# Kernel tuning notes

Hardware: AMD Instinct MI355X
Metric: run time of the kernel (lower is better)

The kernel has to match this reference:

```python
import jax, jax.numpy as jnp
import numpy as np

N = 50000
E = 800000
IN_DIM = 64          # 'in_dim'; ndata h has dim 2*in_dim, p has dim in_dim
EDGE_DIM = 32
OUT_DIM = 64
AVG_D_LOG = 2.8332   # avg_d['log'] = log(avg_degree + 1), avg_degree = 16
EPS_STD = 1e-5
EPS_BN = 1e-5


def setup_inputs() -> dict:
    key = jax.random.key(0)
    ks = jax.random.split(key, 16)
    def glorot(k, fan_in, fan_out):
        lim = np.sqrt(6.0 / (fan_in + fan_out)).astype(np.float32)
        return jax.random.uniform(k, (fan_in, fan_out), jnp.float32, -lim, lim)
    d_pre_h = 2 * 2 * IN_DIM + EDGE_DIM   # 288
    d_pre_p = 2 * IN_DIM + EDGE_DIM       # 160
    d_post_h = (4 * 3 + 2) * IN_DIM       # 896
    d_post_p = (4 * 3 + 1) * IN_DIM       # 832
    return {
        "h": jax.random.normal(ks[0], (N, 2 * IN_DIM), jnp.float32),
        "p": jax.random.normal(ks[1], (N, IN_DIM), jnp.float32),
        "e": jax.random.normal(ks[2], (E, EDGE_DIM), jnp.float32),
        "src": jax.random.randint(ks[3], (E,), 0, N, jnp.int32),
        "dst": jax.random.randint(ks[4], (E,), 0, N, jnp.int32),
        "snorm_n": jax.random.uniform(ks[5], (N, 1), jnp.float32, 0.05, 1.0),
        "W_pre_h": glorot(ks[6], d_pre_h, IN_DIM),
        "b_pre_h": jnp.zeros((IN_DIM,), jnp.float32),
        "W_pre_p": glorot(ks[7], d_pre_p, IN_DIM),
        "b_pre_p": jnp.zeros((IN_DIM,), jnp.float32),
        "W_post_h": glorot(ks[8], d_post_h, OUT_DIM),
        "b_post_h": jnp.zeros((OUT_DIM,), jnp.float32),
        "W_post_p": glorot(ks[9], d_post_p, OUT_DIM),
        "b_post_p": jnp.zeros((OUT_DIM,), jnp.float32),
        "bn_gamma": jnp.ones((OUT_DIM,), jnp.float32),
        "bn_beta": jnp.zeros((OUT_DIM,), jnp.float32),
    }


def _agg_scale(msg, dst, deg):
    # msg: [E, d] edge messages reduced at dst; PNA aggregators mean/max/min/std
    degc = jnp.maximum(deg, 1.0)
    s = jax.ops.segment_sum(msg, dst, num_segments=N)
    mean = s / degc[:, None]
    sq = jax.ops.segment_sum(msg * msg, dst, num_segments=N) / degc[:, None]
    var = jax.nn.relu(sq - mean * mean)
    std = jnp.sqrt(var + EPS_STD)
    has = (deg > 0)[:, None]
    mx = jnp.where(has, jax.ops.segment_max(msg, dst, num_segments=N), 0.0)
    mn = jnp.where(has, jax.ops.segment_min(msg, dst, num_segments=N), 0.0)
    agg = jnp.concatenate([mean, mx, mn, std], axis=1)  # [N, 4d]
    logd = jnp.where(deg > 0, jnp.log(deg + 1.0), 1.0)
    amp = (logd / AVG_D_LOG)[:, None]
    att = (AVG_D_LOG / logd)[:, None]
    # scalers: identity, amplification, attenuation -> [N, 12d]
    return jnp.concatenate([agg, agg * amp, agg * att], axis=1)


def reference(h, p, e, src, dst, snorm_n,
              W_pre_h, b_pre_h, W_pre_p, b_pre_p,
              W_post_h, b_post_h, W_post_p, b_post_p,
              bn_gamma, bn_beta):
    # pretrans (1-layer MLP == linear) on concatenated edge endpoint features
    z_h = jnp.concatenate([h[src], h[dst], e], axis=1)   # [E, 4*in+edge]
    z_p = jnp.concatenate([p[src], p[dst], e], axis=1)   # [E, 2*in+edge]
    e_for_h = z_h @ W_pre_h + b_pre_h                    # [E, in]
    e_for_p = z_p @ W_pre_p + b_pre_p                    # [E, in]

    deg = jax.ops.segment_sum(jnp.ones((E,), jnp.float32), dst, num_segments=N)
    agg_h = _agg_scale(e_for_h, dst, deg)                # [N, 12*in]
    agg_p = _agg_scale(e_for_p, dst, deg)                # [N, 12*in]

    h_cat = jnp.concatenate([h, agg_h], axis=1)          # [N, 14*in]
    p_cat = jnp.concatenate([p, agg_p], axis=1)          # [N, 13*in]
    h_out = h_cat @ W_post_h + b_post_h                  # [N, out]
    p_out = p_cat @ W_post_p + b_post_p                  # [N, out]

    # graph norm
    h_out = h_out * snorm_n
    # batch norm (training-mode batch statistics, biased variance)
    mu = jnp.mean(h_out, axis=0)
    var = jnp.mean((h_out - mu) ** 2, axis=0)
    h_out = (h_out - mu) / jnp.sqrt(var + EPS_BN) * bn_gamma + bn_beta
    # dropout = identity (eval / p=0)
    return h_out, p_out
```

## Files before the change

### kernel.cpp

```cpp
#include <hip/hip_runtime.h>
#include <hip/hip_bf16.h>
#include <hip/hip_fp16.h>


#define N_NODES 50000
#define N_EDGES 800000
#define NS 3200000
#define AVG_D_LOG 2.8332f

typedef unsigned short u16;
typedef unsigned int u32;
typedef __attribute__((ext_vector_type(8))) short short8;
typedef __attribute__((ext_vector_type(4))) float f32x4;

__device__ __forceinline__ float bflo(u32 u) { return __uint_as_float(u << 16); }
__device__ __forceinline__ float bfhi(u32 u) { return __uint_as_float(u & 0xffff0000u); }
__device__ __forceinline__ float bf2f(u16 u) { return __uint_as_float(((u32)u) << 16); }
__device__ __forceinline__ u16 f2bf(float x) {
  u32 u = __float_as_uint(x);
  return (u16)((u + 0x7fff + ((u >> 16) & 1)) >> 16);
}
__device__ __forceinline__ u16 f2h(float x) { return __half_as_ushort(__float2half(x)); }
__device__ __forceinline__ float h2f(u16 x) { return __half2float(__ushort_as_half(x)); }
__device__ __forceinline__ float hlo(u32 u) { return __half2float(__ushort_as_half((u16)(u & 0xffffu))); }
__device__ __forceinline__ float hhi(u32 u) { return __half2float(__ushort_as_half((u16)(u >> 16))); }

__device__ __forceinline__ int is_bf(const void* gamma) {
  return ((const u32*)gamma)[0] == 0x3F803F80u ? 1 : 0;
}

__device__ __forceinline__ f32x4 mfma16(short8 a, short8 b, f32x4 c) {
  return __builtin_amdgcn_mfma_f32_16x16x32_bf16(a, b, c, 0, 0, 0);
}

__device__ __forceinline__ void load8(float z[8], const void* base, size_t off,
                                      int bf) {
  if (bf) {
    uint4 u = *(const uint4*)((const u16*)base + off);
    z[0] = bflo(u.x); z[1] = bfhi(u.x); z[2] = bflo(u.y); z[3] = bfhi(u.y);
    z[4] = bflo(u.z); z[5] = bfhi(u.z); z[6] = bflo(u.w); z[7] = bfhi(u.w);
  } else {
    const float* f = (const float*)base + off;
    float4 a = *(const float4*)f;
    float4 b = *(const float4*)(f + 4);
    z[0] = a.x; z[1] = a.y; z[2] = a.z; z[3] = a.w;
    z[4] = b.x; z[5] = b.y; z[6] = b.z; z[7] = b.w;
  }
}

__device__ __forceinline__ float load1(const void* base, size_t off, int bf) {
  return bf ? bf2f(((const u16*)base)[off]) : ((const float*)base)[off];
}

__global__ __launch_bounds__(256) void k_convert(
    const void* __restrict__ Wpreh, const void* __restrict__ Wprep,
    const void* __restrict__ Wposth, const void* __restrict__ Wpostp,
    const void* __restrict__ bpreh, const void* __restrict__ bprep,
    const void* __restrict__ bposth, const void* __restrict__ bpostp,
    const void* __restrict__ gamma, float* __restrict__ bias,
    u16* __restrict__ frag) {
  int i = blockIdx.x * 256 + threadIdx.x;
  if (i >= 256 + 139264) return;
  int bf = is_bf(gamma);
  if (i < 256) {
    const void* s = (i < 64) ? bpreh : (i < 128) ? bprep : (i < 192) ? bposth : bpostp;
    bias[i] = load1(s, i & 63, bf);
    return;
  }
  int g = i - 256;
  const void* W; int fidx, rowoff;
  if (g < 8192)        { W = Wpreh;  fidx = g;          rowoff = 0; }
  else if (g < 16384)  { W = Wpreh;  fidx = g - 8192;   rowoff = 128; }
  else if (g < 20480)  { W = Wprep;  fidx = g - 16384;  rowoff = 0; }
  else if (g < 24576)  { W = Wprep;  fidx = g - 20480;  rowoff = 64; }
  else if (g < 81920)  { W = Wposth; fidx = g - 24576;  rowoff = 0; }
  else if (g < 135168) { W = Wpostp; fidx = g - 81920;  rowoff = 0; }
  else if (g < 137216) { W = Wpreh;  fidx = g - 135168; rowoff = 256; }
  else                 { W = Wprep;  fidx = g - 137216; rowoff = 128; }
  int f = fidx;
  int kc = f >> 11, nt = (f >> 9) & 3, lane = (f >> 3) & 63, j = f & 7;
  int k = kc * 32 + (lane >> 4) * 8 + j;
  int n = nt * 16 + (lane & 15);
  frag[g] = f2bf(load1(W, (size_t)(rowoff + k) * 64 + n, bf));
}

__global__ __launch_bounds__(256) void k_hist(const int* __restrict__ dst,
                                              int* __restrict__ cnt) {
  int i = blockIdx.x * 256 + threadIdx.x;
  if (i < N_EDGES) atomicAdd(cnt + dst[i], 1);
}

__global__ __launch_bounds__(1024) void k_scan1(const int* __restrict__ cnt,
                                                int* __restrict__ offs,
                                                int* __restrict__ bsum) {
  __shared__ int buf[1024];
  int t = threadIdx.x;
  int i = blockIdx.x * 1024 + t;
  int v = (i < N_NODES) ? cnt[i] : 0;
  buf[t] = v;
  __syncthreads();
#pragma unroll
  for (int d = 1; d < 1024; d <<= 1) {
    int x = (t >= d) ? buf[t - d] : 0;
    __syncthreads();
    buf[t] += x;
    __syncthreads();
  }
  if (i < N_NODES) offs[i] = buf[t] - v;
  if (t == 1023) bsum[blockIdx.x] = buf[1023];
}
__global__ void k_scan2(const int* __restrict__ bsum, int* __restrict__ boff,
                        int* __restrict__ offs, int nb) {
  if (threadIdx.x == 0 && blockIdx.x == 0) {
    int run = 0;
    for (int b = 0; b < nb; ++b) { boff[b] = run; run += bsum[b]; }
    offs[N_NODES] = run;
  }
}
__global__ __launch_bounds__(256) void k_scan3(int* __restrict__ offs,
                                               const int* __restrict__ boff,
                                               int* __restrict__ cnt) {
  int i = blockIdx.x * 256 + threadIdx.x;
  if (i < N_NODES) {
    int v = offs[i] + boff[i >> 10];
    offs[i] = v;
    cnt[i] = v;
  }
}

__global__ __launch_bounds__(256) void k_order(const int* __restrict__ src,
                                               const int* __restrict__ dst,
                                               int* __restrict__ cnt,
                                               int2* __restrict__ epack) {
  int i = blockIdx.x * 256 + threadIdx.x;
  if (i < N_EDGES) {
    int pos = atomicAdd(cnt + dst[i], 1);
    epack[pos] = make_int2(i, src[i]);
  }
}

__global__ __launch_bounds__(256) void k_uproj(
    const void* __restrict__ h, const void* __restrict__ p,
    const float* __restrict__ bias, const u16* __restrict__ frag,
    const void* __restrict__ gamma, u16* __restrict__ Usrc,
    u16* __restrict__ Udst) {
  int wid = (blockIdx.x * 256 + threadIdx.x) >> 6;
  int lane = threadIdx.x & 63;
  if (wid >= 12500) return;
  int part = wid / 3125;
  int node0 = (wid % 3125) * 16;
  int bf = is_bf(gamma);
  const void* feat = (part < 2) ? h : p;
  int pitch = (part < 2) ? 128 : 64;
  int kcn = (part < 2) ? 4 : 2;
  const u16* bfr = frag + (part == 0 ? 0 : part == 1 ? 8192 : part == 2 ? 16384 : 20480);
  u16* U = (part & 1) ? Udst : Usrc;
  int tw = part >> 1;
  int m = lane & 15, quad = lane >> 4;
  f32x4 acc[4];
#pragma unroll
  for (int nt = 0; nt < 4; ++nt) acc[nt] = (f32x4){0.f, 0.f, 0.f, 0.f};
#pragma unroll
  for (int kc = 0; kc < 4; ++kc) {
    if (kc >= kcn) break;
    float z[8];
    load8(z, feat, (size_t)(node0 + m) * pitch + kc * 32 + quad * 8, bf);
    short8 a;
#pragma unroll
    for (int q = 0; q < 8; ++q) a[q] = (short)f2bf(z[q]);
#pragma unroll
    for (int nt = 0; nt < 4; ++nt) {
      short8 b = *(const short8*)(bfr + (size_t)((kc * 4 + nt) * 64 + lane) * 8);
      acc[nt] = mfma16(a, b, acc[nt]);
    }
  }
  const float* bv = (part == 1) ? bias : (part == 3) ? bias + 64 : nullptr;
#pragma unroll
  for (int r = 0; r < 4; ++r) {
    int node = node0 + quad * 4 + r;
#pragma unroll
    for (int nt = 0; nt < 4; ++nt) {
      int col = nt * 16 + m;
      float v = acc[nt][r] + (bv ? bv[col] : 0.f);
      U[(size_t)node * 128 + col * 2 + tw] = f2h(v);
    }
  }
}

template <int BF>
__global__ __launch_bounds__(256, 4) void k_aggf(
    const void* __restrict__ e, const int2* __restrict__ epack,
    const int* __restrict__ offs, const u32* __restrict__ Us32,
    const u32* __restrict__ Ud32, const u16* __restrict__ Wfh,
    const u16* __restrict__ Wfp, const void* __restrict__ gamma,
    u16* __restrict__ Ah, u16* __restrict__ Ap, float* __restrict__ degf) {
  if (is_bf(gamma) != BF) return;
  int n = blockIdx.x * 4 + (threadIdx.x >> 6);
  int lane = threadIdx.x & 63;
  if (n >= N_NODES) return;
  int m = lane & 15, quad = lane >> 4;
  int s = offs[n], epos = offs[n + 1];
  int deg = epos - s;

  short8 bh[4], bp[4];
#pragma unroll
  for (int nt = 0; nt < 4; ++nt) {
    bh[nt] = *(const short8*)(Wfh + (size_t)(nt * 64 + lane) * 8);
    bp[nt] = *(const short8*)(Wfp + (size_t)(nt * 64 + lane) * 8);
  }
  float uhd[4], upd[4];
#pragma unroll
  for (int nt = 0; nt < 4; ++nt) {
    u32 u = Ud32[(size_t)n * 64 + nt * 16 + m];
    uhd[nt] = hlo(u); upd[nt] = hhi(u);
  }
  float hsum[4], hsq[4], hmx[4], hmn[4], psum[4], psq[4], pmx[4], pmn[4];
#pragma unroll
  for (int nt = 0; nt < 4; ++nt) {
    hsum[nt] = hsq[nt] = psum[nt] = psq[nt] = 0.f;
    hmx[nt] = pmx[nt] = -3.4e38f;
    hmn[nt] = pmn[nt] = 3.4e38f;
  }

  for (int c0 = 0; c0 < deg; c0 += 16) {
    int im = s + c0 + m; im = im < epos ? im : epos - 1;
    int eid = epack[im].x;
    int b0 = s + c0 + quad * 4;
    int i0 = b0 < epos ? b0 : epos - 1;
    int i1 = b0 + 1 < epos ? b0 + 1 : epos - 1;
    int i2 = b0 + 2 < epos ? b0 + 2 : epos - 1;
    int i3 = b0 + 3 < epos ? b0 + 3 : epos - 1;
    int sce0 = epack[i0].y, sce1 = epack[i1].y;
    int sce2 = epack[i2].y, sce3 = epack[i3].y;
    u32 usv0[4], usv1[4], usv2[4], usv3[4];
#pragma unroll
    for (int nt = 0; nt < 4; ++nt) {
      usv0[nt] = Us32[(size_t)sce0 * 64 + nt * 16 + m];
      usv1[nt] = Us32[(size_t)sce1 * 64 + nt * 16 + m];
      usv2[nt] = Us32[(size_t)sce2 * 64 + nt * 16 + m];
      usv3[nt] = Us32[(size_t)sce3 * 64 + nt * 16 + m];
    }
    float z[8];
    load8(z, e, (size_t)eid * 32 + quad * 8, BF);
    short8 a;
#pragma unroll
    for (int q = 0; q < 8; ++q) a[q] = (short)f2bf(z[q]);
    bool v0 = (c0 + quad * 4 + 0) < deg;
    bool v1 = (c0 + quad * 4 + 1) < deg;
    bool v2 = (c0 + quad * 4 + 2) < deg;
    bool v3 = (c0 + quad * 4 + 3) < deg;

    {
      f32x4 acc[4];
#pragma unroll
      for (int nt = 0; nt < 4; ++nt)
        acc[nt] = mfma16(a, bh[nt], (f32x4){0.f, 0.f, 0.f, 0.f});
#pragma unroll
      for (int nt = 0; nt < 4; ++nt) {
        float w0 = acc[nt][0] + hlo(usv0[nt]);
        float w1 = acc[nt][1] + hlo(usv1[nt]);
        float w2 = acc[nt][2] + hlo(usv2[nt]);
        float w3 = acc[nt][3] + hlo(usv3[nt]);
        hmx[nt] = fmaxf(fmaxf(hmx[nt], w0), fmaxf(fmaxf(w1, w2), w3));
        hmn[nt] = fminf(fminf(hmn[nt], w0), fminf(fminf(w1, w2), w3));
        float z0 = v0 ? w0 : 0.f, z1 = v1 ? w1 : 0.f;
        float z2 = v2 ? w2 : 0.f, z3 = v3 ? w3 : 0.f;
        hsum[nt] += (z0 + z1) + (z2 + z3);
        hsq[nt] = fmaf(z0, z0, fmaf(z1, z1, fmaf(z2, z2, fmaf(z3, z3, hsq[nt]))));
      }
    }
    {
      f32x4 acc[4];
#pragma unroll
      for (int nt = 0; nt < 4; ++nt)
        acc[nt] = mfma16(a, bp[nt], (f32x4){0.f, 0.f, 0.f, 0.f});
#pragma unroll
      for (int nt = 0; nt < 4; ++nt) {
        float w0 = acc[nt][0] + hhi(usv0[nt]);
        float w1 = acc[nt][1] + hhi(usv1[nt]);
        float w2 = acc[nt][2] + hhi(usv2[nt]);
        float w3 = acc[nt][3] + hhi(usv3[nt]);
        pmx[nt] = fmaxf(fmaxf(pmx[nt], w0), fmaxf(fmaxf(w1, w2), w3));
        pmn[nt] = fminf(fminf(pmn[nt], w0), fminf(fminf(w1, w2), w3));
        float z0 = v0 ? w0 : 0.f, z1 = v1 ? w1 : 0.f;
        float z2 = v2 ? w2 : 0.f, z3 = v3 ? w3 : 0.f;
        psum[nt] += (z0 + z1) + (z2 + z3);
        psq[nt] = fmaf(z0, z0, fmaf(z1, z1, fmaf(z2, z2, fmaf(z3, z3, psq[nt]))));
      }
    }
  }

  float dv = (float)deg;
  bool has = deg > 0;
  float inv = has ? 1.f / dv : 1.f;
  if (lane == 0) degf[n] = dv;

#pragma unroll
  for (int nt = 0; nt < 4; ++nt) {
    hsum[nt] += __shfl_xor(hsum[nt], 16); hsum[nt] += __shfl_xor(hsum[nt], 32);
    hsq[nt] += __shfl_xor(hsq[nt], 16);   hsq[nt] += __shfl_xor(hsq[nt], 32);
    hmx[nt] = fmaxf(hmx[nt], __shfl_xor(hmx[nt], 16));
    hmx[nt] = fmaxf(hmx[nt], __shfl_xor(hmx[nt], 32));
    hmn[nt] = fminf(hmn[nt], __shfl_xor(hmn[nt], 16));
    hmn[nt] = fminf(hmn[nt], __shfl_xor(hmn[nt], 32));
    psum[nt] += __shfl_xor(psum[nt], 16); psum[nt] += __shfl_xor(psum[nt], 32);
    psq[nt] += __shfl_xor(psq[nt], 16);   psq[nt] += __shfl_xor(psq[nt], 32);
    pmx[nt] = fmaxf(pmx[nt], __shfl_xor(pmx[nt], 16));
    pmx[nt] = fmaxf(pmx[nt], __shfl_xor(pmx[nt], 32));
    pmn[nt] = fminf(pmn[nt], __shfl_xor(pmn[nt], 16));
    pmn[nt] = fminf(pmn[nt], __shfl_xor(pmn[nt], 32));
  }

#pragma unroll
  for (int nt = 0; nt < 4; ++nt) {
    {
      float mean_w = hsum[nt] * inv;
      float var = fmaf(-mean_w, mean_w, hsq[nt] * inv);
      var = var > 0.f ? var : 0.f;
      float sd = sqrtf(var + 1e-5f);
      float o = quad == 0 ? (has ? mean_w + uhd[nt] : 0.f)
              : quad == 1 ? (has ? hmx[nt] + uhd[nt] : 0.f)
              : quad == 2 ? (has ? hmn[nt] + uhd[nt] : 0.f) : sd;
      Ah[(size_t)n * 256 + quad * 64 + nt * 16 + m] = f2bf(o);
    }
    {
      float mean_w = psum[nt] * inv;
      float var = fmaf(-mean_w, mean_w, psq[nt] * inv);
      var = var > 0.f ? var : 0.f;
      float sd = sqrtf(var + 1e-5f);
      float o = quad == 0 ? (has ? mean_w + upd[nt] : 0.f)
              : quad == 1 ? (has ? pmx[nt] + upd[nt] : 0.f)
              : quad == 2 ? (has ? pmn[nt] + upd[nt] : 0.f) : sd;
      Ap[(size_t)n * 256 + quad * 64 + nt * 16 + m] = f2bf(o);
    }
  }
}

__global__ __launch_bounds__(256) void k_node(
    const void* __restrict__ h, const void* __restrict__ p,
    const u16* __restrict__ Ah, const u16* __restrict__ Ap,
    const void* __restrict__ snorm, const float* __restrict__ degf,
    const u16* __restrict__ BfH, const u16* __restrict__ BfP,
    const float* __restrict__ biasH, const float* __restrict__ biasP,
    const void* __restrict__ gamma, float* __restrict__ outh,
    float* __restrict__ outp) {
  int w = (blockIdx.x * 256 + threadIdx.x) >> 6;
  int lane = threadIdx.x & 63;
  if (w >= N_NODES / 16) return;
  int bf = is_bf(gamma);
  int m = lane & 15, quad = lane >> 4;
  int node0 = w * 16;

  float ampr[4], attr[4];
#pragma unroll
  for (int r = 0; r < 4; ++r) {
    float dv = degf[node0 + quad * 4 + r];
    float logd = (dv > 0.5f) ? logf(dv + 1.f) : 1.f;
    ampr[r] = logd * (1.f / AVG_D_LOG);
    attr[r] = AVG_D_LOG / logd;
  }

  f32x4 accB[4], accA[4], accT[4];
#pragma unroll
  for (int nt = 0; nt < 4; ++nt) {
    accB[nt] = (f32x4){0.f, 0.f, 0.f, 0.f};
    accA[nt] = (f32x4){0.f, 0.f, 0.f, 0.f};
    accT[nt] = (f32x4){0.f, 0.f, 0.f, 0.f};
  }
#pragma unroll 2
  for (int kc = 0; kc < 12; ++kc) {
    short8 a;
    if (kc < 4) {
      float z[8];
      load8(z, h, (size_t)(node0 + m) * 128 + kc * 32 + quad * 8, bf);
#pragma unroll
      for (int q = 0; q < 8; ++q) a[q] = (short)f2bf(z[q]);
    } else {
      a = *(const short8*)(Ah + (size_t)(node0 + m) * 256 + (kc - 4) * 32 + quad * 8);
    }
#pragma unroll
    for (int nt = 0; nt < 4; ++nt)
      accB[nt] = mfma16(a, *(const short8*)(BfH + (size_t)((kc * 4 + nt) * 64 + lane) * 8), accB[nt]);
    if (kc >= 4) {
      int kk = kc - 4;
#pragma unroll
      for (int nt = 0; nt < 4; ++nt)
        accA[nt] = mfma16(a, *(const short8*)(BfH + 24576 + (size_t)((kk * 4 + nt) * 64 + lane) * 8), accA[nt]);
#pragma unroll
      for (int nt = 0; nt < 4; ++nt)
        accT[nt] = mfma16(a, *(const short8*)(BfH + 40960 + (size_t)((kk * 4 + nt) * 64 + lane) * 8), accT[nt]);
    }
  }
  float bH[4];
#pragma unroll
  for (int nt = 0; nt < 4; ++nt) bH[nt] = biasH[nt * 16 + m];
#pragma unroll
  for (int r = 0; r < 4; ++r) {
    int node = node0 + quad * 4 + r;
    float sn = load1(snorm, node, bf);
#pragma unroll
    for (int nt = 0; nt < 4; ++nt) {
      float v = accB[nt][r] + ampr[r] * accA[nt][r] + attr[r] * accT[nt][r] + bH[nt];
      outh[(size_t)node * 64 + nt * 16 + m] = v * sn;
    }
  }

#pragma unroll
  for (int nt = 0; nt < 4; ++nt) {
    accB[nt] = (f32x4){0.f, 0.f, 0.f, 0.f};
    accA[nt] = (f32x4){0.f, 0.f, 0.f, 0.f};
    accT[nt] = (f32x4){0.f, 0.f, 0.f, 0.f};
  }
#pragma unroll 2
  for (int kc = 0; kc < 10; ++kc) {
    short8 a;
    if (kc < 2) {
      float z[8];
      load8(z, p, (size_t)(node0 + m) * 64 + kc * 32 + quad * 8, bf);
#pragma unroll
      for (int q = 0; q < 8; ++q) a[q] = (short)f2bf(z[q]);
    } else {
      a = *(const short8*)(Ap + (size_t)(node0 + m) * 256 + (kc - 2) * 32 + quad * 8);
    }
#pragma unroll
    for (int nt = 0; nt < 4; ++nt)
      accB[nt] = mfma16(a, *(const short8*)(BfP + (size_t)((kc * 4 + nt) * 64 + lane) * 8), accB[nt]);
    if (kc >= 2) {
      int kk = kc - 2;
#pragma unroll
      for (int nt = 0; nt < 4; ++nt)
        accA[nt] = mfma16(a, *(const short8*)(BfP + 20480 + (size_t)((kk * 4 + nt) * 64 + lane) * 8), accA[nt]);
#pragma unroll
      for (int nt = 0; nt < 4; ++nt)
        accT[nt] = mfma16(a, *(const short8*)(BfP + 36864 + (size_t)((kk * 4 + nt) * 64 + lane) * 8), accT[nt]);
    }
  }
  float bP[4];
#pragma unroll
  for (int nt = 0; nt < 4; ++nt) bP[nt] = biasP[nt * 16 + m];
#pragma unroll
  for (int r = 0; r < 4; ++r) {
    int node = node0 + quad * 4 + r;
#pragma unroll
    for (int nt = 0; nt < 4; ++nt) {
      float v = accB[nt][r] + ampr[r] * accA[nt][r] + attr[r] * accT[nt][r] + bP[nt];
      outp[(size_t)node * 64 + nt * 16 + m] = v;
    }
  }
}

__global__ __launch_bounds__(256) void k_bnstats(const float* __restrict__ hpre,
                                                 float* __restrict__ bnacc) {
  int j = threadIdx.x & 63;
  float s = 0.0f, q = 0.0f;
  for (int n = blockIdx.x * 4 + (threadIdx.x >> 6); n < N_NODES;
       n += gridDim.x * 4) {
    float x = hpre[(size_t)n * 64 + j];
    s += x; q += x * x;
  }
  __shared__ float ls[256], lq[256];
  ls[threadIdx.x] = s; lq[threadIdx.x] = q;
  __syncthreads();
  if (threadIdx.x < 64) {
    s = ls[threadIdx.x] + ls[threadIdx.x + 64] + ls[threadIdx.x + 128] + ls[threadIdx.x + 192];
    q = lq[threadIdx.x] + lq[threadIdx.x + 64] + lq[threadIdx.x + 128] + lq[threadIdx.x + 192];
    atomicAdd(bnacc + threadIdx.x, s);
    atomicAdd(bnacc + 64 + threadIdx.x, q);
  }
}

__global__ __launch_bounds__(256) void k_bnapply(
    float* __restrict__ outh, const float* __restrict__ bnacc,
    const void* __restrict__ gamma, const void* __restrict__ beta) {
  int i = blockIdx.x * 256 + threadIdx.x;
  if (i >= NS) return;
  int bf = is_bf(gamma);
  int j = i & 63;
  const float invN = 1.0f / (float)N_NODES;
  float mu = bnacc[j] * invN;
  float var = fmaf(-mu, mu, bnacc[64 + j] * invN);
  var = var > 0.0f ? var : 0.0f;
  float sc = load1(gamma, j, bf) * rsqrtf(var + 1e-5f);
  float sh = load1(beta, j, bf) - mu * sc;
  outh[i] = fmaf(outh[i], sc, sh);
}

extern "C" void kernel_launch(void* const* d_in, const int* in_sizes, int n_in,
                              void* d_out, int out_size, void* d_ws,
                              size_t ws_size, hipStream_t stream) {
  const void* h = d_in[0];
  const void* p = d_in[1];
  const void* e = d_in[2];
  const int* src = (const int*)d_in[3];
  const int* dst = (const int*)d_in[4];
  const void* snorm = d_in[5];
  const void* Wpreh = d_in[6];
  const void* bpreh = d_in[7];
  const void* Wprep = d_in[8];
  const void* bprep = d_in[9];
  const void* Wposth = d_in[10];
  const void* bposth = d_in[11];
  const void* Wpostp = d_in[12];
  const void* bpostp = d_in[13];
  const void* gamma = d_in[14];
  const void* beta = d_in[15];

  float* ws = (float*)d_ws;
  u16* Usrc = (u16*)ws;
  u16* Udst = (u16*)(ws + 3200000L);
  u16* Ah = (u16*)(ws + 6400000L);
  u16* Ap = (u16*)(ws + 12800000L);
  int2* epack = (int2*)(ws + 19200000L);
  int* cnt = (int*)(ws + 20800016L);
  int* offs = (int*)(ws + 20850016L);
  float* degf = ws + 20900020L;
  int* bsum = (int*)(ws + 20950020L);
  int* boff = (int*)(ws + 20950084L);
  float* bnacc = ws + 20950148L;
  float* bias = ws + 20950276L;
  u16* frag = (u16*)(ws + 20950532L);

  u16* fragPostH = frag + 24576;
  u16* fragPostP = frag + 81920;
  u16* fragWehF = frag + 135168;
  u16* fragWepF = frag + 137216;

  float* outh = (float*)d_out;
  float* outp = outh + (size_t)NS;

  int bfh = -1;
  if (in_sizes && n_in >= 16) {
    if (in_sizes[0] == 25600000) bfh = 0;
    else if (in_sizes[0] == 12800000) bfh = 1;
  }

  hipMemsetAsync(cnt, 0, N_NODES * sizeof(int), stream);
  hipMemsetAsync(bnacc, 0, 128 * sizeof(float), stream);
  k_convert<<<(256 + 139264 + 255) / 256, 256, 0, stream>>>(
      Wpreh, Wprep, Wposth, Wpostp, bpreh, bprep, bposth, bpostp, gamma, bias,
      frag);
  k_hist<<<(N_EDGES + 255) / 256, 256, 0, stream>>>(dst, cnt);
  const int NB = (N_NODES + 1023) / 1024;
  k_scan1<<<NB, 1024, 0, stream>>>(cnt, offs, bsum);
  k_scan2<<<1, 64, 0, stream>>>(bsum, boff, offs, NB);
  k_scan3<<<(N_NODES + 255) / 256, 256, 0, stream>>>(offs, boff, cnt);
  k_order<<<(N_EDGES + 255) / 256, 256, 0, stream>>>(src, dst, cnt, epack);
  k_uproj<<<(12500 + 3) / 4, 256, 0, stream>>>(h, p, bias, frag, gamma, Usrc,
                                               Udst);
  if (bfh != 1)
    k_aggf<0><<<(N_NODES + 3) / 4, 256, 0, stream>>>(
        e, epack, offs, (const u32*)Usrc, (const u32*)Udst, fragWehF, fragWepF,
        gamma, Ah, Ap, degf);
  if (bfh != 0)
    k_aggf<1><<<(N_NODES + 3) / 4, 256, 0, stream>>>(
        e, epack, offs, (const u32*)Usrc, (const u32*)Udst, fragWehF, fragWepF,
        gamma, Ah, Ap, degf);
  k_node<<<(N_NODES / 16 + 3) / 4, 256, 0, stream>>>(
      h, p, Ah, Ap, snorm, degf, fragPostH, fragPostP, bias + 128, bias + 192,
      gamma, outh, outp);
  k_bnstats<<<256, 256, 0, stream>>>(outh, bnacc);
  k_bnapply<<<(NS + 255) / 256, 256, 0, stream>>>(outh, bnacc, gamma, beta);
}
```

Before: 513.6 us.

## Fuse memsets and scan passes, merge h/p projections, split full edge chunks

Several changes land together. Zeroing of counts and BN accumulators moves into the weight-convert kernel, and the three-kernel scan becomes a single-block scan. The U projection computes the h and p halves in one wave and writes packed half2 words. The aggregation kernel gives each wave two nodes, handles full 16-edge chunks without clamping or masking, and loads bf16 edge features directly. Together these cut launch count and per-edge overhead, but the single-block scan runs serially on one block and the paired-node waves may lose some occupancy balance.

```diff
diff --git a/kernel.cpp b/kernel.cpp
--- a/kernel.cpp
+++ b/kernel.cpp
@@ -20,8 +20,6 @@
   u32 u = __float_as_uint(x);
   return (u16)((u + 0x7fff + ((u >> 16) & 1)) >> 16);
 }
-__device__ __forceinline__ u16 f2h(float x) { return __half_as_ushort(__float2half(x)); }
-__device__ __forceinline__ float h2f(u16 x) { return __half2float(__ushort_as_half(x)); }
 __device__ __forceinline__ float hlo(u32 u) { return __half2float(__ushort_as_half((u16)(u & 0xffffu))); }
 __device__ __forceinline__ float hhi(u32 u) { return __half2float(__ushort_as_half((u16)(u >> 16))); }
 
@@ -52,15 +50,35 @@
   return bf ? bf2f(((const u16*)base)[off]) : ((const float*)base)[off];
 }
 
+__device__ __forceinline__ short8 cvt8bf(const float z[8]) {
+  union { __hip_bfloat162 b[4]; short8 s; } u;
+  u.b[0] = __float22bfloat162_rn(make_float2(z[0], z[1]));
+  u.b[1] = __float22bfloat162_rn(make_float2(z[2], z[3]));
+  u.b[2] = __float22bfloat162_rn(make_float2(z[4], z[5]));
+  u.b[3] = __float22bfloat162_rn(make_float2(z[6], z[7]));
+  return u.s;
+}
+
+__device__ __forceinline__ u32 packh2(float a, float b) {
+  union { __half2 h; u32 u; } x;
+  x.h = __float22half2_rn(make_float2(a, b));
+  return x.u;
+}
+
 __global__ __launch_bounds__(256) void k_convert(
     const void* __restrict__ Wpreh, const void* __restrict__ Wprep,
     const void* __restrict__ Wposth, const void* __restrict__ Wpostp,
     const void* __restrict__ bpreh, const void* __restrict__ bprep,
     const void* __restrict__ bposth, const void* __restrict__ bpostp,
     const void* __restrict__ gamma, float* __restrict__ bias,
-    u16* __restrict__ frag) {
+    u16* __restrict__ frag, int* __restrict__ cnt, float* __restrict__ bnacc) {
   int i = blockIdx.x * 256 + threadIdx.x;
-  if (i >= 256 + 139264) return;
+  if (i >= 256 + 139264) {
+    int z = i - (256 + 139264);
+    if (z < N_NODES) cnt[z] = 0;
+    else if (z < N_NODES + 128) bnacc[z - N_NODES] = 0.0f;
+    return;
+  }
   int bf = is_bf(gamma);
   if (i < 256) {
     const void* s = (i < 64) ? bpreh : (i < 128) ? bprep : (i < 192) ? bposth : bpostp;
@@ -90,51 +108,49 @@
   if (i < N_EDGES) atomicAdd(cnt + dst[i], 1);
 }
 
-__global__ __launch_bounds__(1024) void k_scan1(const int* __restrict__ cnt,
-                                                int* __restrict__ offs,
-                                                int* __restrict__ bsum) {
-  __shared__ int buf[1024];
+__global__ __launch_bounds__(1024) void k_scan(const int* __restrict__ cnt,
+                                               int* __restrict__ offs,
+                                               int* __restrict__ cur) {
+  __shared__ int part[1024];
+  const int CH = 49;
   int t = threadIdx.x;
-  int i = blockIdx.x * 1024 + t;
-  int v = (i < N_NODES) ? cnt[i] : 0;
-  buf[t] = v;
+  int base = t * CH;
+  int sum = 0;
+#pragma unroll 7
+  for (int j = 0; j < CH; ++j) {
+    int idx = base + j;
+    sum += (idx < N_NODES) ? cnt[idx] : 0;
+  }
+  part[t] = sum;
   __syncthreads();
 #pragma unroll
   for (int d = 1; d < 1024; d <<= 1) {
-    int x = (t >= d) ? buf[t - d] : 0;
+    int x = (t >= d) ? part[t - d] : 0;
     __syncthreads();
-    buf[t] += x;
+    part[t] += x;
     __syncthreads();
   }
-  if (i < N_NODES) offs[i] = buf[t] - v;
-  if (t == 1023) bsum[blockIdx.x] = buf[1023];
-}
-__global__ void k_scan2(const int* __restrict__ bsum, int* __restrict__ boff,
-                        int* __restrict__ offs, int nb) {
-  if (threadIdx.x == 0 && blockIdx.x == 0) {
-    int run = 0;
-    for (int b = 0; b < nb; ++b) { boff[b] = run; run += bsum[b]; }
-    offs[N_NODES] = run;
-  }
-}
-__global__ __launch_bounds__(256) void k_scan3(int* __restrict__ offs,
-                                               const int* __restrict__ boff,
-                                               int* __restrict__ cnt) {
-  int i = blockIdx.x * 256 + threadIdx.x;
-  if (i < N_NODES) {
-    int v = offs[i] + boff[i >> 10];
-    offs[i] = v;
-    cnt[i] = v;
-  }
+  int run = part[t] - sum;
+#pragma unroll 7
+  for (int j = 0; j < CH; ++j) {
+    int idx = base + j;
+    if (idx < N_NODES) {
+      int c = cnt[idx];
+      offs[idx] = run;
+      cur[idx] = run;
+      run += c;
+    }
+  }
+  if (t == 1023) offs[N_NODES] = run;
 }
 
 __global__ __launch_bounds__(256) void k_order(const int* __restrict__ src,
                                                const int* __restrict__ dst,
-                                               int* __restrict__ cnt,
+                                               int* __restrict__ cur,
                                                int2* __restrict__ epack) {
   int i = blockIdx.x * 256 + threadIdx.x;
   if (i < N_EDGES) {
-    int pos = atomicAdd(cnt + dst[i], 1);
+    int pos = atomicAdd(cur + dst[i], 1);
     epack[pos] = make_int2(i, src[i]);
   }
 }
@@ -142,47 +158,55 @@
 __global__ __launch_bounds__(256) void k_uproj(
     const void* __restrict__ h, const void* __restrict__ p,
     const float* __restrict__ bias, const u16* __restrict__ frag,
-    const void* __restrict__ gamma, u16* __restrict__ Usrc,
-    u16* __restrict__ Udst) {
+    const void* __restrict__ gamma, u32* __restrict__ Usrc,
+    u32* __restrict__ Udst) {
   int wid = (blockIdx.x * 256 + threadIdx.x) >> 6;
   int lane = threadIdx.x & 63;
-  if (wid >= 12500) return;
+  if (wid >= 6250) return;
   int part = wid / 3125;
   int node0 = (wid % 3125) * 16;
   int bf = is_bf(gamma);
-  const void* feat = (part < 2) ? h : p;
-  int pitch = (part < 2) ? 128 : 64;
-  int kcn = (part < 2) ? 4 : 2;
-  const u16* bfr = frag + (part == 0 ? 0 : part == 1 ? 8192 : part == 2 ? 16384 : 20480);
-  u16* U = (part & 1) ? Udst : Usrc;
-  int tw = part >> 1;
+  const u16* bfrH = frag + (part ? 8192 : 0);
+  const u16* bfrP = frag + (part ? 20480 : 16384);
+  u32* U = part ? Udst : Usrc;
   int m = lane & 15, quad = lane >> 4;
-  f32x4 acc[4];
-#pragma unroll
-  for (int nt = 0; nt < 4; ++nt) acc[nt] = (f32x4){0.f, 0.f, 0.f, 0.f};
+  f32x4 accH[4], accP[4];
+#pragma unroll
+  for (int nt = 0; nt < 4; ++nt) {
+    accH[nt] = (f32x4){0.f, 0.f, 0.f, 0.f};
+    accP[nt] = (f32x4){0.f, 0.f, 0.f, 0.f};
+  }
 #pragma unroll
   for (int kc = 0; kc < 4; ++kc) {
-    if (kc >= kcn) break;
     float z[8];
-    load8(z, feat, (size_t)(node0 + m) * pitch + kc * 32 + quad * 8, bf);
-    short8 a;
-#pragma unroll
-    for (int q = 0; q < 8; ++q) a[q] = (short)f2bf(z[q]);
-#pragma unroll
-    for (int nt = 0; nt < 4; ++nt) {
-      short8 b = *(const short8*)(bfr + (size_t)((kc * 4 + nt) * 64 + lane) * 8);
-      acc[nt] = mfma16(a, b, acc[nt]);
-    }
-  }
-  const float* bv = (part == 1) ? bias : (part == 3) ? bias + 64 : nullptr;
+    load8(z, h, (size_t)(node0 + m) * 128 + kc * 32 + quad * 8, bf);
+    short8 a = cvt8bf(z);
+#pragma unroll
+    for (int nt = 0; nt < 4; ++nt) {
+      short8 b = *(const short8*)(bfrH + (size_t)((kc * 4 + nt) * 64 + lane) * 8);
+      accH[nt] = mfma16(a, b, accH[nt]);
+    }
+  }
+#pragma unroll
+  for (int kc = 0; kc < 2; ++kc) {
+    float z[8];
+    load8(z, p, (size_t)(node0 + m) * 64 + kc * 32 + quad * 8, bf);
+    short8 a = cvt8bf(z);
+#pragma unroll
+    for (int nt = 0; nt < 4; ++nt) {
+      short8 b = *(const short8*)(bfrP + (size_t)((kc * 4 + nt) * 64 + lane) * 8);
+      accP[nt] = mfma16(a, b, accP[nt]);
+    }
+  }
 #pragma unroll
   for (int r = 0; r < 4; ++r) {
     int node = node0 + quad * 4 + r;
 #pragma unroll
     for (int nt = 0; nt < 4; ++nt) {
       int col = nt * 16 + m;
-      float v = acc[nt][r] + (bv ? bv[col] : 0.f);
-      U[(size_t)node * 128 + col * 2 + tw] = f2h(v);
+      float vh = accH[nt][r] + (part ? bias[col] : 0.f);
+      float vp = accP[nt][r] + (part ? bias[64 + col] : 0.f);
+      U[(size_t)node * 64 + col] = packh2(vh, vp);
     }
   }
 }
@@ -195,12 +219,9 @@
     const u16* __restrict__ Wfp, const void* __restrict__ gamma,
     u16* __restrict__ Ah, u16* __restrict__ Ap, float* __restrict__ degf) {
   if (is_bf(gamma) != BF) return;
-  int n = blockIdx.x * 4 + (threadIdx.x >> 6);
+  int n0 = blockIdx.x * 8 + ((threadIdx.x >> 6) << 1);
   int lane = threadIdx.x & 63;
-  if (n >= N_NODES) return;
   int m = lane & 15, quad = lane >> 4;
-  int s = offs[n], epos = offs[n + 1];
-  int deg = epos - s;
 
   short8 bh[4], bp[4];
 #pragma unroll
@@ -208,130 +229,197 @@
     bh[nt] = *(const short8*)(Wfh + (size_t)(nt * 64 + lane) * 8);
     bp[nt] = *(const short8*)(Wfp + (size_t)(nt * 64 + lane) * 8);
   }
-  float uhd[4], upd[4];
-#pragma unroll
-  for (int nt = 0; nt < 4; ++nt) {
-    u32 u = Ud32[(size_t)n * 64 + nt * 16 + m];
-    uhd[nt] = hlo(u); upd[nt] = hhi(u);
-  }
-  float hsum[4], hsq[4], hmx[4], hmn[4], psum[4], psq[4], pmx[4], pmn[4];
-#pragma unroll
-  for (int nt = 0; nt < 4; ++nt) {
-    hsum[nt] = hsq[nt] = psum[nt] = psq[nt] = 0.f;
-    hmx[nt] = pmx[nt] = -3.4e38f;
-    hmn[nt] = pmn[nt] = 3.4e38f;
-  }
-
-  for (int c0 = 0; c0 < deg; c0 += 16) {
-    int im = s + c0 + m; im = im < epos ? im : epos - 1;
-    int eid = epack[im].x;
-    int b0 = s + c0 + quad * 4;
-    int i0 = b0 < epos ? b0 : epos - 1;
-    int i1 = b0 + 1 < epos ? b0 + 1 : epos - 1;
-    int i2 = b0 + 2 < epos ? b0 + 2 : epos - 1;
-    int i3 = b0 + 3 < epos ? b0 + 3 : epos - 1;
-    int sce0 = epack[i0].y, sce1 = epack[i1].y;
-    int sce2 = epack[i2].y, sce3 = epack[i3].y;
-    u32 usv0[4], usv1[4], usv2[4], usv3[4];
-#pragma unroll
-    for (int nt = 0; nt < 4; ++nt) {
-      usv0[nt] = Us32[(size_t)sce0 * 64 + nt * 16 + m];
-      usv1[nt] = Us32[(size_t)sce1 * 64 + nt * 16 + m];
-      usv2[nt] = Us32[(size_t)sce2 * 64 + nt * 16 + m];
-      usv3[nt] = Us32[(size_t)sce3 * 64 + nt * 16 + m];
-    }
-    float z[8];
-    load8(z, e, (size_t)eid * 32 + quad * 8, BF);
-    short8 a;
-#pragma unroll
-    for (int q = 0; q < 8; ++q) a[q] = (short)f2bf(z[q]);
-    bool v0 = (c0 + quad * 4 + 0) < deg;
-    bool v1 = (c0 + quad * 4 + 1) < deg;
-    bool v2 = (c0 + quad * 4 + 2) < deg;
-    bool v3 = (c0 + quad * 4 + 3) < deg;
-
-    {
-      f32x4 acc[4];
-#pragma unroll
-      for (int nt = 0; nt < 4; ++nt)
-        acc[nt] = mfma16(a, bh[nt], (f32x4){0.f, 0.f, 0.f, 0.f});
+
+  for (int nn = 0; nn < 2; ++nn) {
+    int n = n0 + nn;
+    if (n >= N_NODES) return;
+    int s = offs[n], epos = offs[n + 1];
+    int deg = epos - s;
+    float uhd[4], upd[4];
+#pragma unroll
+    for (int nt = 0; nt < 4; ++nt) {
+      u32 u = Ud32[(size_t)n * 64 + nt * 16 + m];
+      uhd[nt] = hlo(u); upd[nt] = hhi(u);
+    }
+    float hsum[4], hsq[4], hmx[4], hmn[4], psum[4], psq[4], pmx[4], pmn[4];
+#pragma unroll
+    for (int nt = 0; nt < 4; ++nt) {
+      hsum[nt] = hsq[nt] = psum[nt] = psq[nt] = 0.f;
+      hmx[nt] = pmx[nt] = -3.4e38f;
+      hmn[nt] = pmn[nt] = 3.4e38f;
+    }
+
+    int full = deg & ~15;
+    int c0 = 0;
+    for (; c0 < full; c0 += 16) {
+      int eid = epack[s + c0 + m].x;
+      int b0 = s + c0 + quad * 4;
+      int sce0 = epack[b0].y, sce1 = epack[b0 + 1].y;
+      int sce2 = epack[b0 + 2].y, sce3 = epack[b0 + 3].y;
+      u32 usv0[4], usv1[4], usv2[4], usv3[4];
 #pragma unroll
       for (int nt = 0; nt < 4; ++nt) {
-        float w0 = acc[nt][0] + hlo(usv0[nt]);
-        float w1 = acc[nt][1] + hlo(usv1[nt]);
-        float w2 = acc[nt][2] + hlo(usv2[nt]);
-        float w3 = acc[nt][3] + hlo(usv3[nt]);
-        hmx[nt] = fmaxf(fmaxf(hmx[nt], w0), fmaxf(fmaxf(w1, w2), w3));
-        hmn[nt] = fminf(fminf(hmn[nt], w0), fminf(fminf(w1, w2), w3));
-        float z0 = v0 ? w0 : 0.f, z1 = v1 ? w1 : 0.f;
-        float z2 = v2 ? w2 : 0.f, z3 = v3 ? w3 : 0.f;
-        hsum[nt] += (z0 + z1) + (z2 + z3);
-        hsq[nt] = fmaf(z0, z0, fmaf(z1, z1, fmaf(z2, z2, fmaf(z3, z3, hsq[nt]))));
-      }
-    }
-    {
-      f32x4 acc[4];
-#pragma unroll
-      for (int nt = 0; nt < 4; ++nt)
-        acc[nt] = mfma16(a, bp[nt], (f32x4){0.f, 0.f, 0.f, 0.f});
+        usv0[nt] = Us32[(size_t)sce0 * 64 + nt * 16 + m];
+        usv1[nt] = Us32[(size_t)sce1 * 64 + nt * 16 + m];
+        usv2[nt] = Us32[(size_t)sce2 * 64 + nt * 16 + m];
+        usv3[nt] = Us32[(size_t)sce3 * 64 + nt * 16 + m];
+      }
+      short8 a;
+      if (BF) {
+        a = *(const short8*)((const u16*)e + (size_t)eid * 32 + quad * 8);
+      } else {
+        float z[8];
+        load8(z, e, (size_t)eid * 32 + quad * 8, 0);
+        a = cvt8bf(z);
+      }
+      {
+        f32x4 acc[4];
+#pragma unroll
+        for (int nt = 0; nt < 4; ++nt)
+          acc[nt] = mfma16(a, bh[nt], (f32x4){0.f, 0.f, 0.f, 0.f});
+#pragma unroll
+        for (int nt = 0; nt < 4; ++nt) {
+          float w0 = acc[nt][0] + hlo(usv0[nt]);
+          float w1 = acc[nt][1] + hlo(usv1[nt]);
+          float w2 = acc[nt][2] + hlo(usv2[nt]);
+          float w3 = acc[nt][3] + hlo(usv3[nt]);
+          hmx[nt] = fmaxf(fmaxf(hmx[nt], w0), fmaxf(fmaxf(w1, w2), w3));
+          hmn[nt] = fminf(fminf(hmn[nt], w0), fminf(fminf(w1, w2), w3));
+          hsum[nt] += (w0 + w1) + (w2 + w3);
+          hsq[nt] = fmaf(w0, w0, fmaf(w1, w1, fmaf(w2, w2, fmaf(w3, w3, hsq[nt]))));
+        }
+      }
+      {
+        f32x4 acc[4];
+#pragma unroll
+        for (int nt = 0; nt < 4; ++nt)
+          acc[nt] = mfma16(a, bp[nt], (f32x4){0.f, 0.f, 0.f, 0.f});
+#pragma unroll
+        for (int nt = 0; nt < 4; ++nt) {
+          float w0 = acc[nt][0] + hhi(usv0[nt]);
+          float w1 = acc[nt][1] + hhi(usv1[nt]);
+          float w2 = acc[nt][2] + hhi(usv2[nt]);
+          float w3 = acc[nt][3] + hhi(usv3[nt]);
+          pmx[nt] = fmaxf(fmaxf(pmx[nt], w0), fmaxf(fmaxf(w1, w2), w3));
+          pmn[nt] = fminf(fminf(pmn[nt], w0), fminf(fminf(w1, w2), w3));
+          psum[nt] += (w0 + w1) + (w2 + w3);
+          psq[nt] = fmaf(w0, w0, fmaf(w1, w1, fmaf(w2, w2, fmaf(w3, w3, psq[nt]))));
+        }
+      }
+    }
+    if (c0 < deg) {
+      int im = s + c0 + m; im = im < epos ? im : epos - 1;
+      int eid = epack[im].x;
+      int b0 = s + c0 + quad * 4;
+      int i0 = b0 < epos ? b0 : epos - 1;
+      int i1 = b0 + 1 < epos ? b0 + 1 : epos - 1;
+      int i2 = b0 + 2 < epos ? b0 + 2 : epos - 1;
+      int i3 = b0 + 3 < epos ? b0 + 3 : epos - 1;
+      int sce0 = epack[i0].y, sce1 = epack[i1].y;
+      int sce2 = epack[i2].y, sce3 = epack[i3].y;
+      u32 usv0[4], usv1[4], usv2[4], usv3[4];
 #pragma unroll
       for (int nt = 0; nt < 4; ++nt) {
-        float w0 = acc[nt][0] + hhi(usv0[nt]);
-        float w1 = acc[nt][1] + hhi(usv1[nt]);
-        float w2 = acc[nt][2] + hhi(usv2[nt]);
-        float w3 = acc[nt][3] + hhi(usv3[nt]);
-        pmx[nt] = fmaxf(fmaxf(pmx[nt], w0), fmaxf(fmaxf(w1, w2), w3));
-        pmn[nt] = fminf(fminf(pmn[nt], w0), fminf(fminf(w1, w2), w3));
-        float z0 = v0 ? w0 : 0.f, z1 = v1 ? w1 : 0.f;
-        float z2 = v2 ? w2 : 0.f, z3 = v3 ? w3 : 0.f;
-        psum[nt] += (z0 + z1) + (z2 + z3);
-        psq[nt] = fmaf(z0, z0, fmaf(z1, z1, fmaf(z2, z2, fmaf(z3, z3, psq[nt]))));
-      }
-    }
-  }
-
-  float dv = (float)deg;
-  bool has = deg > 0;
-  float inv = has ? 1.f / dv : 1.f;
-  if (lane == 0) degf[n] = dv;
-
-#pragma unroll
-  for (int nt = 0; nt < 4; ++nt) {
-    hsum[nt] += __shfl_xor(hsum[nt], 16); hsum[nt] += __shfl_xor(hsum[nt], 32);
-    hsq[nt] += __shfl_xor(hsq[nt], 16);   hsq[nt] += __shfl_xor(hsq[nt], 32);
-    hmx[nt] = fmaxf(hmx[nt], __shfl_xor(hmx[nt], 16));
-    hmx[nt] = fmaxf(hmx[nt], __shfl_xor(hmx[nt], 32));
-    hmn[nt] = fminf(hmn[nt], __shfl_xor(hmn[nt], 16));
-    hmn[nt] = fminf(hmn[nt], __shfl_xor(hmn[nt], 32));
-    psum[nt] += __shfl_xor(psum[nt], 16); psum[nt] += __shfl_xor(psum[nt], 32);
-    psq[nt] += __shfl_xor(psq[nt], 16);   psq[nt] += __shfl_xor(psq[nt], 32);
-    pmx[nt] = fmaxf(pmx[nt], __shfl_xor(pmx[nt], 16));
-    pmx[nt] = fmaxf(pmx[nt], __shfl_xor(pmx[nt], 32));
-    pmn[nt] = fminf(pmn[nt], __shfl_xor(pmn[nt], 16));
-    pmn[nt] = fminf(pmn[nt], __shfl_xor(pmn[nt], 32));
-  }
-
-#pragma unroll
-  for (int nt = 0; nt < 4; ++nt) {
-    {
-      float mean_w = hsum[nt] * inv;
-      float var = fmaf(-mean_w, mean_w, hsq[nt] * inv);
-      var = var > 0.f ? var : 0.f;
-      float sd = sqrtf(var + 1e-5f);
-      float o = quad == 0 ? (has ? mean_w + uhd[nt] : 0.f)
-              : quad == 1 ? (has ? hmx[nt] + uhd[nt] : 0.f)
-              : quad == 2 ? (has ? hmn[nt] + uhd[nt] : 0.f) : sd;
-      Ah[(size_t)n * 256 + quad * 64 + nt * 16 + m] = f2bf(o);
-    }
-    {
-      float mean_w = psum[nt] * inv;
-      float var = fmaf(-mean_w, mean_w, psq[nt] * inv);
-      var = var > 0.f ? var : 0.f;
-      float sd = sqrtf(var + 1e-5f);
-      float o = quad == 0 ? (has ? mean_w + upd[nt] : 0.f)
-              : quad == 1 ? (has ? pmx[nt] + upd[nt] : 0.f)
-              : quad == 2 ? (has ? pmn[nt] + upd[nt] : 0.f) : sd;
-      Ap[(size_t)n * 256 + quad * 64 + nt * 16 + m] = f2bf(o);
+        usv0[nt] = Us32[(size_t)sce0 * 64 + nt * 16 + m];
+        usv1[nt] = Us32[(size_t)sce1 * 64 + nt * 16 + m];
+        usv2[nt] = Us32[(size_t)sce2 * 64 + nt * 16 + m];
+        usv3[nt] = Us32[(size_t)sce3 * 64 + nt * 16 + m];
+      }
+      short8 a;
+      if (BF) {
+        a = *(const short8*)((const u16*)e + (size_t)eid * 32 + quad * 8);
+      } else {
+        float z[8];
+        load8(z, e, (size_t)eid * 32 + quad * 8, 0);
+        a = cvt8bf(z);
+      }
+      bool v0 = (c0 + quad * 4 + 0) < deg;
+      bool v1 = (c0 + quad * 4 + 1) < deg;
+      bool v2 = (c0 + quad * 4 + 2) < deg;
+      bool v3 = (c0 + quad * 4 + 3) < deg;
+      {
+        f32x4 acc[4];
+#pragma unroll
+        for (int nt = 0; nt < 4; ++nt)
+          acc[nt] = mfma16(a, bh[nt], (f32x4){0.f, 0.f, 0.f, 0.f});
+#pragma unroll
+        for (int nt = 0; nt < 4; ++nt) {
+          float w0 = acc[nt][0] + hlo(usv0[nt]);
+          float w1 = acc[nt][1] + hlo(usv1[nt]);
+          float w2 = acc[nt][2] + hlo(usv2[nt]);
+          float w3 = acc[nt][3] + hlo(usv3[nt]);
+          hmx[nt] = fmaxf(fmaxf(hmx[nt], w0), fmaxf(fmaxf(w1, w2), w3));
+          hmn[nt] = fminf(fminf(hmn[nt], w0), fminf(fminf(w1, w2), w3));
+          float z0 = v0 ? w0 : 0.f, z1 = v1 ? w1 : 0.f;
+          float z2 = v2 ? w2 : 0.f, z3 = v3 ? w3 : 0.f;
+          hsum[nt] += (z0 + z1) + (z2 + z3);
+          hsq[nt] = fmaf(z0, z0, fmaf(z1, z1, fmaf(z2, z2, fmaf(z3, z3, hsq[nt]))));
+        }
+      }
+      {
+        f32x4 acc[4];
+#pragma unroll
+        for (int nt = 0; nt < 4; ++nt)
+          acc[nt] = mfma16(a, bp[nt], (f32x4){0.f, 0.f, 0.f, 0.f});
+#pragma unroll
+        for (int nt = 0; nt < 4; ++nt) {
+          float w0 = acc[nt][0] + hhi(usv0[nt]);
+          float w1 = acc[nt][1] + hhi(usv1[nt]);
+          float w2 = acc[nt][2] + hhi(usv2[nt]);
+          float w3 = acc[nt][3] + hhi(usv3[nt]);
+          pmx[nt] = fmaxf(fmaxf(pmx[nt], w0), fmaxf(fmaxf(w1, w2), w3));
+          pmn[nt] = fminf(fminf(pmn[nt], w0), fminf(fminf(w1, w2), w3));
+          float z0 = v0 ? w0 : 0.f, z1 = v1 ? w1 : 0.f;
+          float z2 = v2 ? w2 : 0.f, z3 = v3 ? w3 : 0.f;
+          psum[nt] += (z0 + z1) + (z2 + z3);
+          psq[nt] = fmaf(z0, z0, fmaf(z1, z1, fmaf(z2, z2, fmaf(z3, z3, psq[nt]))));
+        }
+      }
+    }
+
+    float dv = (float)deg;
+    bool has = deg > 0;
+    float inv = has ? 1.f / dv : 1.f;
+    if (lane == 0) degf[n] = dv;
+
+#pragma unroll
+    for (int nt = 0; nt < 4; ++nt) {
+      hsum[nt] += __shfl_xor(hsum[nt], 16); hsum[nt] += __shfl_xor(hsum[nt], 32);
+      hsq[nt] += __shfl_xor(hsq[nt], 16);   hsq[nt] += __shfl_xor(hsq[nt], 32);
+      hmx[nt] = fmaxf(hmx[nt], __shfl_xor(hmx[nt], 16));
+      hmx[nt] = fmaxf(hmx[nt], __shfl_xor(hmx[nt], 32));
+      hmn[nt] = fminf(hmn[nt], __shfl_xor(hmn[nt], 16));
+      hmn[nt] = fminf(hmn[nt], __shfl_xor(hmn[nt], 32));
+      psum[nt] += __shfl_xor(psum[nt], 16); psum[nt] += __shfl_xor(psum[nt], 32);
+      psq[nt] += __shfl_xor(psq[nt], 16);   psq[nt] += __shfl_xor(psq[nt], 32);
+      pmx[nt] = fmaxf(pmx[nt], __shfl_xor(pmx[nt], 16));
+      pmx[nt] = fmaxf(pmx[nt], __shfl_xor(pmx[nt], 32));
+      pmn[nt] = fminf(pmn[nt], __shfl_xor(pmn[nt], 16));
+      pmn[nt] = fminf(pmn[nt], __shfl_xor(pmn[nt], 32));
+    }
+
+#pragma unroll
+    for (int nt = 0; nt < 4; ++nt) {
+      {
+        float mean_w = hsum[nt] * inv;
+        float var = fmaf(-mean_w, mean_w, hsq[nt] * inv);
+        var = var > 0.f ? var : 0.f;
+        float sd = sqrtf(var + 1e-5f);
+        float o = quad == 0 ? (has ? mean_w + uhd[nt] : 0.f)
+                : quad == 1 ? (has ? hmx[nt] + uhd[nt] : 0.f)
+                : quad == 2 ? (has ? hmn[nt] + uhd[nt] : 0.f) : sd;
+        Ah[(size_t)n * 256 + quad * 64 + nt * 16 + m] = f2bf(o);
+      }
+      {
+        float mean_w = psum[nt] * inv;
+        float var = fmaf(-mean_w, mean_w, psq[nt] * inv);
+        var = var > 0.f ? var : 0.f;
+        float sd = sqrtf(var + 1e-5f);
+        float o = quad == 0 ? (has ? mean_w + upd[nt] : 0.f)
+                : quad == 1 ? (has ? pmx[nt] + upd[nt] : 0.f)
+                : quad == 2 ? (has ? pmn[nt] + upd[nt] : 0.f) : sd;
+        Ap[(size_t)n * 256 + quad * 64 + nt * 16 + m] = f2bf(o);
+      }
     }
   }
 }
@@ -373,8 +461,7 @@
     if (kc < 4) {
       float z[8];
       load8(z, h, (size_t)(node0 + m) * 128 + kc * 32 + quad * 8, bf);
-#pragma unroll
-      for (int q = 0; q < 8; ++q) a[q] = (short)f2bf(z[q]);
+      a = cvt8bf(z);
     } else {
       a = *(const short8*)(Ah + (size_t)(node0 + m) * 256 + (kc - 4) * 32 + quad * 8);
     }
@@ -417,8 +504,7 @@
     if (kc < 2) {
       float z[8];
       load8(z, p, (size_t)(node0 + m) * 64 + kc * 32 + quad * 8, bf);
-#pragma unroll
-      for (int q = 0; q < 8; ++q) a[q] = (short)f2bf(z[q]);
+      a = cvt8bf(z);
     } else {
       a = *(const short8*)(Ap + (size_t)(node0 + m) * 256 + (kc - 2) * 32 + quad * 8);
     }
@@ -506,19 +592,18 @@
   const void* beta = d_in[15];
 
   float* ws = (float*)d_ws;
-  u16* Usrc = (u16*)ws;
-  u16* Udst = (u16*)(ws + 3200000L);
+  u32* Usrc = (u32*)ws;
+  u32* Udst = (u32*)(ws + 3200000L);
   u16* Ah = (u16*)(ws + 6400000L);
   u16* Ap = (u16*)(ws + 12800000L);
   int2* epack = (int2*)(ws + 19200000L);
   int* cnt = (int*)(ws + 20800016L);
   int* offs = (int*)(ws + 20850016L);
   float* degf = ws + 20900020L;
-  int* bsum = (int*)(ws + 20950020L);
-  int* boff = (int*)(ws + 20950084L);
-  float* bnacc = ws + 20950148L;
-  float* bias = ws + 20950276L;
-  u16* frag = (u16*)(ws + 20950532L);
+  int* cur = (int*)(ws + 20950020L);
+  float* bnacc = ws + 21000020L;
+  float* bias = ws + 21000148L;
+  u16* frag = (u16*)(ws + 21000404L);
 
   u16* fragPostH = frag + 24576;
   u16* fragPostP = frag + 81920;
@@ -534,27 +619,20 @@
     else if (in_sizes[0] == 12800000) bfh = 1;
   }
 
-  hipMemsetAsync(cnt, 0, N_NODES * sizeof(int), stream);
-  hipMemsetAsync(bnacc, 0, 128 * sizeof(float), stream);
-  k_convert<<<(256 + 139264 + 255) / 256, 256, 0, stream>>>(
+  k_convert<<<(256 + 139264 + N_NODES + 128 + 255) / 256, 256, 0, stream>>>(
       Wpreh, Wprep, Wposth, Wpostp, bpreh, bprep, bposth, bpostp, gamma, bias,
-      frag);
+      frag, cnt, bnacc);
   k_hist<<<(N_EDGES + 255) / 256, 256, 0, stream>>>(dst, cnt);
-  const int NB = (N_NODES + 1023) / 1024;
-  k_scan1<<<NB, 1024, 0, stream>>>(cnt, offs, bsum);
-  k_scan2<<<1, 64, 0, stream>>>(bsum, boff, offs, NB);
-  k_scan3<<<(N_NODES + 255) / 256, 256, 0, stream>>>(offs, boff, cnt);
-  k_order<<<(N_EDGES + 255) / 256, 256, 0, stream>>>(src, dst, cnt, epack);
-  k_uproj<<<(12500 + 3) / 4, 256, 0, stream>>>(h, p, bias, frag, gamma, Usrc,
-                                               Udst);
+  k_scan<<<1, 1024, 0, stream>>>(cnt, offs, cur);
+  k_order<<<(N_EDGES + 255) / 256, 256, 0, stream>>>(src, dst, cur, epack);
+  k_uproj<<<(6250 + 3) / 4, 256, 0, stream>>>(h, p, bias, frag, gamma, Usrc,
+                                              Udst);
   if (bfh != 1)
-    k_aggf<0><<<(N_NODES + 3) / 4, 256, 0, stream>>>(
-        e, epack, offs, (const u32*)Usrc, (const u32*)Udst, fragWehF, fragWepF,
-        gamma, Ah, Ap, degf);
+    k_aggf<0><<<(N_NODES + 7) / 8, 256, 0, stream>>>(
+        e, epack, offs, Usrc, Udst, fragWehF, fragWepF, gamma, Ah, Ap, degf);
   if (bfh != 0)
-    k_aggf<1><<<(N_NODES + 3) / 4, 256, 0, stream>>>(
-        e, epack, offs, (const u32*)Usrc, (const u32*)Udst, fragWehF, fragWepF,
-        gamma, Ah, Ap, degf);
+    k_aggf<1><<<(N_NODES + 7) / 8, 256, 0, stream>>>(
+        e, epack, offs, Usrc, Udst, fragWehF, fragWepF, gamma, Ah, Ap, degf);
   k_node<<<(N_NODES / 16 + 3) / 4, 256, 0, stream>>>(
       h, p, Ah, Ap, snorm, degf, fragPostH, fragPostP, bias + 128, bias + 192,
       gamma, outh, outp);
```

New measurement: 644.1 us. 25.4% more time.
